# Optimization experiments

Measured on AMD Instinct MI355X. Metric: run time of the kernel, lower is better.

## Reference

```python
import jax, jax.numpy as jnp
import numpy as np

H = 32          # num query heads
KV = 8          # num kv heads
D = 64          # head_dim
WIN = 512       # sliding_window
BASE = 10000.0  # rope base


def setup_inputs() -> dict:
    key = jax.random.key(0)
    ks = jax.random.split(key, 5)
    B, S, DIM = 2, 2048, 2048
    x = jax.random.normal(ks[0], (B, S, DIM), dtype=jnp.float32)
    wq = jax.random.normal(ks[1], (H * D, DIM), dtype=jnp.float32) * 0.02
    wk = jax.random.normal(ks[2], (KV * D, DIM), dtype=jnp.float32) * 0.02
    wv = jax.random.normal(ks[3], (KV * D, DIM), dtype=jnp.float32) * 0.02
    wo = jax.random.normal(ks[4], (DIM, H * D), dtype=jnp.float32) * 0.02
    return {"x": x, "wq": wq, "wk": wk, "wv": wv, "wo": wo}


def _rope_tables(S):
    inv_freq = 1.0 / (BASE ** (jnp.arange(0, D, 2, dtype=jnp.float32) / D))
    t = jnp.arange(S, dtype=jnp.float32)
    freqs = t[:, None] * inv_freq[None, :]          # [S, D/2]
    emb = jnp.concatenate([freqs, freqs], axis=-1)  # [S, D]
    return jnp.cos(emb)[:, None, :], jnp.sin(emb)[:, None, :]  # [S,1,D]


def _rotate_half(u):
    return jnp.concatenate([-u[..., D // 2:], u[..., :D // 2]], axis=-1)


def reference(x, wq, wk, wv, wo):
    B, S, _ = x.shape
    q = (x @ wq.T).reshape(B, S, H, D)
    k = (x @ wk.T).reshape(B, S, KV, D)
    v = (x @ wv.T).reshape(B, S, KV, D)

    cos, sin = _rope_tables(S)  # [S,1,D] broadcasts over batch and heads
    q = q * cos + _rotate_half(q) * sin
    k = k * cos + _rotate_half(k) * sin

    q = q.transpose(0, 2, 1, 3)                        # [B,H,S,D]
    k = jnp.repeat(k.transpose(0, 2, 1, 3), H // KV, axis=1)  # [B,H,S,D]
    v = jnp.repeat(v.transpose(0, 2, 1, 3), H // KV, axis=1)

    scale = 1.0 / jnp.sqrt(jnp.float32(D))
    scores = jnp.einsum('bhqd,bhkd->bhqk', q, k) * scale  # [B,H,S,S]

    i = jnp.arange(S)[:, None]
    j = jnp.arange(S)[None, :]
    window_mask = jnp.abs(i - j) > WIN // 2   # True = masked (outside window)
    causal_mask = j > i                        # True = masked (future)
    masked = window_mask | causal_mask
    scores = jnp.where(masked[None, None], -jnp.inf, scores)

    attn = jax.nn.softmax(scores, axis=-1)
    out = jnp.einsum('bhqk,bhkd->bhqd', attn, v)  # [B,H,S,D]
    out = out.transpose(0, 2, 1, 3).reshape(B, S, H * D)
    return out @ wo.T
```

## Files before the change

kernel.cpp:

```cpp
#include <hip/hip_runtime.h>
#include <cstdint>
#include <cstddef>

#define SLEN 2048
#define NB 2
#define NH 32
#define NKV 8
#define HD 64
#define MROWS 4096
#define QDIM 2048
#define KVDIM 512
#define WINH 256

typedef float f32x4 __attribute__((ext_vector_type(4)));
typedef __bf16 bf16x8 __attribute__((ext_vector_type(8)));

__device__ __forceinline__ unsigned short f2bf(float f) {
  union { float f; unsigned u; } v; v.f = f;
  unsigned r = v.u + 0x7fffu + ((v.u >> 16) & 1u);
  return (unsigned short)(r >> 16);
}
__device__ __forceinline__ float bf2f(unsigned short h) {
  union { unsigned u; float f; } v; v.u = ((unsigned)h) << 16;
  return v.f;
}
__device__ __forceinline__ unsigned pk2(float a, float b) {
  return (unsigned)f2bf(a) | ((unsigned)f2bf(b) << 16);
}
__device__ __forceinline__ unsigned cvtpk(float a, float b) {
  unsigned r;
  asm("v_cvt_pk_bf16_f32 %0, %1, %2" : "=v"(r) : "v"(a), "v"(b));
  return r;
}
__device__ __forceinline__ uint4 cvt16(float4 a, float4 b) {
  uint4 u;
  u.x = pk2(a.x, a.y); u.y = pk2(a.z, a.w);
  u.z = pk2(b.x, b.y); u.w = pk2(b.z, b.w);
  return u;
}
__device__ __forceinline__ void async16(const unsigned short* g, unsigned short* l) {
  __builtin_amdgcn_global_load_lds(
      (const __attribute__((address_space(1))) unsigned int*)g,
      (__attribute__((address_space(3))) unsigned int*)l, 16, 0, 0);
}

__global__ void rope_table(float2* __restrict__ tab) {
  int tid = blockIdx.x * 256 + threadIdx.x;
  int d = tid & 31;
  int s = tid >> 5;
  float inv = expf((float)d * (-2.0f / 64.0f) * 9.210340371976184f);
  float ang = (float)s * inv;
  float sn, cs;
  sincosf(ang, &sn, &cs);
  tab[tid] = make_float2(cs, sn);
}

__global__ void conv_xw(const float* __restrict__ x,
                        const float* __restrict__ wq, const float* __restrict__ wk,
                        const float* __restrict__ wv,
                        unsigned short* __restrict__ xb, unsigned short* __restrict__ wqkvb) {
  size_t t = (size_t)blockIdx.x * 256 + threadIdx.x;
  if (t < (size_t)1048576) {
    size_t e = t * 8;
    float4 a = *(const float4*)(x + e);
    float4 b = *(const float4*)(x + e + 4);
    *(uint4*)(xb + e) = cvt16(a, b);
  } else {
    size_t e = (t - 1048576) * 8;
    int row = (int)(e >> 11);
    const float* src; size_t off;
    if (row < 2048)       { src = wq; off = e; }
    else if (row < 2560)  { src = wk; off = e - (size_t)2048 * 2048; }
    else                  { src = wv; off = e - (size_t)2560 * 2048; }
    float4 a = *(const float4*)(src + off);
    float4 b = *(const float4*)(src + off + 4);
    *(uint4*)(wqkvb + e) = cvt16(a, b);
  }
}

__global__ void conv_bf16(const float* __restrict__ src, unsigned short* __restrict__ dst) {
  size_t t = (size_t)blockIdx.x * 256 + threadIdx.x;
  float4 a = *(const float4*)(src + t * 8);
  float4 b = *(const float4*)(src + t * 8 + 4);
  *(uint4*)(dst + t * 8) = cvt16(a, b);
}

__global__ void rope_qk(unsigned short* __restrict__ qb,
                        unsigned short* __restrict__ kb,
                        const float* __restrict__ tabf) {
  const float2* tab = (const float2*)tabf;
  int tid = blockIdx.x * 256 + threadIdx.x;
  int oct = tid & 3;
  int head = (tid >> 2) % 40;
  int row = tid / 160;
  int s = row & (SLEN - 1);
  int d0 = oct * 8;
  unsigned short* p = (head < NH)
      ? qb + (size_t)row * QDIM + head * HD
      : kb + (size_t)row * KVDIM + (head - NH) * HD;
  uint4 u0 = *(const uint4*)(p + d0);
  uint4 u1 = *(const uint4*)(p + d0 + 32);
  const unsigned short* a16 = (const unsigned short*)&u0;
  const unsigned short* b16 = (const unsigned short*)&u1;
  unsigned short o0[8], o1[8];
#pragma unroll
  for (int j = 0; j < 8; ++j) {
    float2 cs = tab[s * 32 + d0 + j];
    float a = bf2f(a16[j]), b = bf2f(b16[j]);
    o0[j] = f2bf(a * cs.x - b * cs.y);
    o1[j] = f2bf(b * cs.x + a * cs.y);
  }
  *(uint4*)(p + d0)      = *(const uint4*)o0;
  *(uint4*)(p + d0 + 32) = *(const uint4*)o1;
}

__global__ __launch_bounds__(512, 2) void qkv_gemm(
    const unsigned short* __restrict__ Ap, const unsigned short* __restrict__ Bp,
    unsigned short* __restrict__ o_q, unsigned short* __restrict__ o_k,
    unsigned short* __restrict__ o_v)
{
  extern __shared__ unsigned short L[];
  constexpr int NT = 32;

  const int bid = blockIdx.x;
  const int swz = (bid & 7) * 32 + (bid >> 3);
  const int bm0 = (swz & 15) * 256;
  const int bn0 = (swz >> 4) * 192;

  const int tid = threadIdx.x;
  const int lane = tid & 63, wid = tid >> 6;
  const int g = lane >> 4, cl = lane & 15;
  const int wm = wid >> 2, wn = wid & 3;

  const int r0 = wid * 32 + (lane >> 2);
  const int s0 = (((lane & 3) ^ ((lane >> 3) & 3)) << 3);
  const unsigned short* gA = Ap + (size_t)(bm0 + r0) * 2048 + s0;
  const unsigned short* gB = Bp + (size_t)(bn0 + r0) * 2048 + s0;

  const int slotus = ((g ^ ((cl >> 1) & 3)) << 3);
  const int aread = (wm * 128 + cl) * 32 + slotus;
  const int bread = (wn * 48 + cl) * 32 + slotus;

#define REG_(b, op, kh) ((((b) * 2 + (op)) * 2 + (kh)) * 8192)
#define STG(op, kh, tt, db) do { \
    const unsigned short* s_ = ((op) ? gB : gA) + (tt) * 64 + (kh) * 32; \
    unsigned short* d_ = L + REG_(db, op, kh) + wid * 1024; \
    async16(s_, d_); \
    async16(s_ + 16 * 2048, d_ + 512); \
  } while (0)
#define LDA(dst, kh, mh) \
    _Pragma("unroll") for (int mf = 0; mf < 4; ++mf) \
      dst[mf] = *(const bf16x8*)&L[REG_(cb, 0, kh) + aread + (mh) * 2048 + mf * 512];
#define LDB(dst, kh) \
    _Pragma("unroll") for (int nf = 0; nf < 3; ++nf) \
      dst[nf] = *(const bf16x8*)&L[REG_(cb, 1, kh) + bread + nf * 512];
#define MM(mh, A, B) do { \
    __builtin_amdgcn_s_setprio(1); \
    _Pragma("unroll") for (int mf = 0; mf < 4; ++mf) \
      _Pragma("unroll") for (int nf = 0; nf < 3; ++nf) \
        acc[(mh) * 4 + mf][nf] = __builtin_amdgcn_mfma_f32_16x16x32_bf16( \
            A[mf], B[nf], acc[(mh) * 4 + mf][nf], 0, 0, 0); \
    __builtin_amdgcn_s_setprio(0); \
  } while (0)

  f32x4 acc[8][3] = {};

  STG(0, 0, 0, 0); STG(1, 0, 0, 0); STG(0, 1, 0, 0); STG(1, 1, 0, 0);
  STG(0, 0, 1, 1); STG(1, 0, 1, 1);
  asm volatile("s_waitcnt vmcnt(4)" ::: "memory");
  __builtin_amdgcn_s_barrier();
  __builtin_amdgcn_sched_barrier(0);

#pragma unroll 1
  for (int t = 0; t < NT; ++t) {
    const int cb = t & 1, nb = cb ^ 1;
    bf16x8 a00[4], a10[4], a01[4], a11[4], b0[3], b1[3];

    if (t + 1 < NT) STG(0, 1, t + 1, nb);
    LDA(a00, 0, 0); LDB(b0, 0);
    if (t + 1 < NT) STG(1, 1, t + 1, nb);
    LDA(a10, 0, 1);
    MM(0, a00, b0);
    LDA(a01, 1, 0); LDB(b1, 1);
    MM(1, a10, b0);
    asm volatile("s_waitcnt lgkmcnt(0)" ::: "memory");
    __builtin_amdgcn_s_barrier();
    __builtin_amdgcn_sched_barrier(0);
    if (t + 2 < NT) STG(0, 0, t + 2, cb);
    LDA(a11, 1, 1);
    MM(0, a01, b1);
    if (t + 2 < NT) STG(1, 0, t + 2, cb);
    MM(1, a11, b1);
    if (t + 2 < NT) { asm volatile("s_waitcnt vmcnt(4)" ::: "memory"); }
    else            { asm volatile("s_waitcnt vmcnt(0)" ::: "memory"); }
    asm volatile("s_waitcnt lgkmcnt(0)" ::: "memory");
    __builtin_amdgcn_s_barrier();
    __builtin_amdgcn_sched_barrier(0);
  }
#undef MM
#undef LDB
#undef LDA
#undef STG
#undef REG_

  const int rb = bm0 + wm * 128;
#pragma unroll
  for (int m = 0; m < 8; ++m)
#pragma unroll
    for (int nf = 0; nf < 3; ++nf) {
      const int col = bn0 + wn * 48 + nf * 16 + cl;
      if (col < QDIM) {
#pragma unroll
        for (int p = 0; p < 4; ++p) {
          int row = rb + m * 16 + g * 4 + p;
          o_q[(size_t)row * QDIM + col] = f2bf(acc[m][nf][p]);
        }
      } else if (col < QDIM + KVDIM) {
#pragma unroll
        for (int p = 0; p < 4; ++p) {
          int row = rb + m * 16 + g * 4 + p;
          o_k[(size_t)row * KVDIM + col - QDIM] = f2bf(acc[m][nf][p]);
        }
      } else {
        int vc = col - QDIM - KVDIM;
        int kvh = vc >> 6, d = vc & 63;
        int row0 = rb + m * 16 + g * 4;
        int bb = row0 >> 11, s = row0 & (SLEN - 1);
        unsigned short* dst = o_v + (((size_t)(bb * NKV + kvh) * HD + d) << 11) + s;
        uint2 u;
        u.x = pk2(acc[m][nf][0], acc[m][nf][1]);
        u.y = pk2(acc[m][nf][2], acc[m][nf][3]);
        *(uint2*)dst = u;
      }
    }
}

__global__ __launch_bounds__(512, 2) void out_gemm(
    const unsigned short* __restrict__ Ap, const unsigned short* __restrict__ Bp,
    float* __restrict__ o_f)
{
  extern __shared__ unsigned short L[];
  constexpr int NT = 32;

  const int bid = blockIdx.x;
  const int swz = (bid & 7) * 32 + (bid >> 3);
  const int bm0 = (swz & 31) * 128;
  const int bn0 = (swz >> 5) * 256;

  const int tid = threadIdx.x;
  const int lane = tid & 63, wid = tid >> 6;
  const int g = lane >> 4, cl = lane & 15;
  const int wm = wid >> 2, wn = wid & 3;

  const int s0 = (((lane & 3) ^ ((lane >> 3) & 3)) << 3);
  const unsigned short* gA = Ap + (size_t)(bm0 + wid * 16 + (lane >> 2)) * 2048 + s0;
  const unsigned short* gB = Bp + (size_t)(bn0 + wid * 32 + (lane >> 2)) * 2048 + s0;

  const int slotus = ((g ^ ((cl >> 1) & 3)) << 3);
  const int aread = (wm * 64 + cl) * 32 + slotus;
  const int bread = (wn * 64 + cl) * 32 + slotus;

#define REGA_(b, kh) ((b) * 24576 + (kh) * 4096)
#define REGB_(b, kh) ((b) * 24576 + 8192 + (kh) * 8192)
#define STGA(kh, tt, db) \
    async16(gA + (tt) * 64 + (kh) * 32, L + REGA_(db, kh) + wid * 512)
#define STGB(kh, tt, db) do { \
    const unsigned short* s_ = gB + (tt) * 64 + (kh) * 32; \
    unsigned short* d_ = L + REGB_(db, kh) + wid * 1024; \
    async16(s_, d_); \
    async16(s_ + 16 * 2048, d_ + 512); \
  } while (0)
#define LA(dst, kh, mp) \
    _Pragma("unroll") for (int mf = 0; mf < 2; ++mf) \
      dst[mf] = *(const bf16x8*)&L[REGA_(cb, kh) + aread + (mp) * 1024 + mf * 512];
#define LB(dst, kh) \
    _Pragma("unroll") for (int nf = 0; nf < 4; ++nf) \
      dst[nf] = *(const bf16x8*)&L[REGB_(cb, kh) + bread + nf * 512];
#define MMO(mp, A, B) do { \
    __builtin_amdgcn_s_setprio(1); \
    _Pragma("unroll") for (int mf = 0; mf < 2; ++mf) \
      _Pragma("unroll") for (int nf = 0; nf < 4; ++nf) \
        acc[(mp) * 2 + mf][nf] = __builtin_amdgcn_mfma_f32_16x16x32_bf16( \
            A[mf], B[nf], acc[(mp) * 2 + mf][nf], 0, 0, 0); \
    __builtin_amdgcn_s_setprio(0); \
  } while (0)

  f32x4 acc[4][4] = {};

  STGA(0, 0, 0); STGB(0, 0, 0); STGA(1, 0, 0); STGB(1, 0, 0);
  STGA(0, 1, 1); STGB(0, 1, 1);
  asm volatile("s_waitcnt vmcnt(3)" ::: "memory");
  __builtin_amdgcn_s_barrier();
  __builtin_amdgcn_sched_barrier(0);

#pragma unroll 1
  for (int t = 0; t < NT; ++t) {
    const int cb = t & 1, nb = cb ^ 1;
    bf16x8 p00[2], p10[2], p01[2], p11[2], b0[4], b1[4];

    if (t + 1 < NT) STGA(1, t + 1, nb);
    LA(p00, 0, 0); LB(b0, 0);
    if (t + 1 < NT) STGB(1, t + 1, nb);
    LA(p10, 0, 1);
    MMO(0, p00, b0);
    LA(p01, 1, 0); LB(b1, 1);
    MMO(1, p10, b0);
    asm volatile("s_waitcnt lgkmcnt(0)" ::: "memory");
    __builtin_amdgcn_s_barrier();
    __builtin_amdgcn_sched_barrier(0);
    if (t + 2 < NT) STGA(0, t + 2, cb);
    LA(p11, 1, 1);
    MMO(0, p01, b1);
    if (t + 2 < NT) STGB(0, t + 2, cb);
    MMO(1, p11, b1);
    if (t + 2 < NT) { asm volatile("s_waitcnt vmcnt(3)" ::: "memory"); }
    else            { asm volatile("s_waitcnt vmcnt(0)" ::: "memory"); }
    asm volatile("s_waitcnt lgkmcnt(0)" ::: "memory");
    __builtin_amdgcn_s_barrier();
    __builtin_amdgcn_sched_barrier(0);
  }
#undef MMO
#undef LB
#undef LA
#undef STGB
#undef STGA
#undef REGB_
#undef REGA_

  const int rb = bm0 + wm * 64;
  const int colb = bn0 + wn * 64;
#pragma unroll
  for (int m = 0; m < 4; ++m)
#pragma unroll
    for (int nf = 0; nf < 4; ++nf)
#pragma unroll
      for (int p = 0; p < 4; ++p) {
        int row = rb + m * 16 + g * 4 + p;
        o_f[(size_t)row * 2048 + colb + nf * 16 + cl] = acc[m][nf][p];
      }
}

__global__ __launch_bounds__(256) void attn(
    const unsigned short* __restrict__ qb, const unsigned short* __restrict__ kb,
    const unsigned short* __restrict__ vt, unsigned short* __restrict__ ao)
{
  __shared__ __align__(16) unsigned short Plds[4][2][16][40];
  const int lane = threadIdx.x & 63, wid = threadIdx.x >> 6;
  const int g = lane >> 4, cl = lane & 15;
  const int qt = blockIdx.x * 4 + wid;
  const int bh = qt >> 6, tl = qt & 63;
  const int i0 = tl * 32;
  const int b = bh >> 5, h = bh & 31, kvh = (bh & 31) >> 2;
  const int qi0 = i0 + cl, qi1 = i0 + 16 + cl;

  const unsigned short* qp0 = qb + ((size_t)(b * SLEN + qi0) * NH + h) * HD + g * 8;
  const unsigned short* qp1 = qb + ((size_t)(b * SLEN + qi1) * NH + h) * HD + g * 8;
  bf16x8 qf00 = *(const bf16x8*)qp0, qf01 = *(const bf16x8*)(qp0 + 32);
  bf16x8 qf10 = *(const bf16x8*)qp1, qf11 = *(const bf16x8*)(qp1 + 32);

  const unsigned short* kbase = kb + ((size_t)b * SLEN * NKV + kvh) * HD + g * 8;
  const unsigned short* vbase = vt + ((size_t)(b * NKV + kvh) * HD) * SLEN;

  f32x4 acc0[4] = {}, acc1[4] = {};
  float m0 = -1e30f, l0 = 0.f, m1 = -1e30f, l1 = 0.f;
  const int jb = (i0 > WINH) ? (i0 - WINH) : 0;

#define LOADK(dst, jj) do { \
    _Pragma("unroll") for (int t = 0; t < 2; ++t) { \
      int krow = (jj) + 16 * t + cl; \
      if (krow > SLEN - 1) krow = SLEN - 1; \
      const unsigned short* kp_ = kbase + (size_t)krow * KVDIM; \
      dst[t * 2]     = *(const bf16x8*)kp_; \
      dst[t * 2 + 1] = *(const bf16x8*)(kp_ + 32); \
    } \
  } while (0)

#define LOADV(dst, jj) do { \
    int jv = (jj) + g * 8; \
    if (jv > SLEN - 8) jv = SLEN - 8; \
    _Pragma("unroll") for (int vb2 = 0; vb2 < 4; ++vb2) \
      dst[vb2] = *(const bf16x8*)(vbase + (size_t)(vb2 * 16 + cl) * SLEN + jv); \
  } while (0)

#define SOFTMAX(SAC, MR, LR, ACC, QI, QF) do { \
    float sm[2][4]; float mx = -1e30f; \
    _Pragma("unroll") for (int t = 0; t < 2; ++t) \
      _Pragma("unroll") for (int p = 0; p < 4; ++p) { \
        int kj = j0 + 16 * t + 4 * g + p; \
        bool ok = (kj <= (QI)) && ((QI) - kj <= WINH); \
        float v = ok ? SAC[t][p] * 0.125f : -1e30f; \
        sm[t][p] = v; mx = fmaxf(mx, v); \
      } \
    mx = fmaxf(mx, __shfl_xor(mx, 16)); \
    mx = fmaxf(mx, __shfl_xor(mx, 32)); \
    float mnew = fmaxf(MR, mx); \
    float corr = __expf(MR - mnew); \
    float ps = 0.f; unsigned pw00, pw01, pw10, pw11; \
    { \
      float p0 = __expf(sm[0][0] - mnew), p1 = __expf(sm[0][1] - mnew); \
      float p2 = __expf(sm[0][2] - mnew), p3 = __expf(sm[0][3] - mnew); \
      ps += p0 + p1 + p2 + p3; pw00 = cvtpk(p0, p1); pw01 = cvtpk(p2, p3); \
      float p4 = __expf(sm[1][0] - mnew), p5 = __expf(sm[1][1] - mnew); \
      float p6 = __expf(sm[1][2] - mnew), p7 = __expf(sm[1][3] - mnew); \
      ps += p4 + p5 + p6 + p7; pw10 = cvtpk(p4, p5); pw11 = cvtpk(p6, p7); \
    } \
    ps += __shfl_xor(ps, 16); ps += __shfl_xor(ps, 32); \
    LR = LR * corr + ps; MR = mnew; \
    _Pragma("unroll") for (int vb2 = 0; vb2 < 4; ++vb2) \
      _Pragma("unroll") for (int p = 0; p < 4; ++p) ACC[vb2][p] *= corr; \
    *(unsigned*)&Plds[wid][QF][cl][4 * g]          = pw00; \
    *(unsigned*)&Plds[wid][QF][cl][4 * g + 2]      = pw01; \
    *(unsigned*)&Plds[wid][QF][cl][16 + 4 * g]     = pw10; \
    *(unsigned*)&Plds[wid][QF][cl][16 + 4 * g + 2] = pw11; \
  } while (0)

#define BODY(KC, KN, VC, VN) do { \
    LOADK(KN, j0 + 32);                           \
    LOADV(VN, j0 + 32);                           \
    f32x4 s0[2], s1[2]; \
    _Pragma("unroll") for (int t = 0; t < 2; ++t) { \
      f32x4 z = {}; \
      z = __builtin_amdgcn_mfma_f32_16x16x32_bf16(KC[t * 2], qf00, z, 0, 0, 0); \
      z = __builtin_amdgcn_mfma_f32_16x16x32_bf16(KC[t * 2 + 1], qf01, z, 0, 0, 0); \
      s0[t] = z; \
      f32x4 z2 = {}; \
      z2 = __builtin_amdgcn_mfma_f32_16x16x32_bf16(KC[t * 2], qf10, z2, 0, 0, 0); \
      z2 = __builtin_amdgcn_mfma_f32_16x16x32_bf16(KC[t * 2 + 1], qf11, z2, 0, 0, 0); \
      s1[t] = z2; \
    } \
    SOFTMAX(s0, m0, l0, acc0, qi0, 0); \
    SOFTMAX(s1, m1, l1, acc1, qi1, 1); \
    bf16x8 pf0 = *(const bf16x8*)&Plds[wid][0][cl][g * 8]; \
    bf16x8 pf1 = *(const bf16x8*)&Plds[wid][1][cl][g * 8]; \
    _Pragma("unroll") for (int vb2 = 0; vb2 < 4; ++vb2) \
      acc0[vb2] = __builtin_amdgcn_mfma_f32_16x16x32_bf16(VC[vb2], pf0, acc0[vb2], 0, 0, 0); \
    _Pragma("unroll") for (int vb2 = 0; vb2 < 4; ++vb2) \
      acc1[vb2] = __builtin_amdgcn_mfma_f32_16x16x32_bf16(VC[vb2], pf1, acc1[vb2], 0, 0, 0); \
  } while (0)

  bf16x8 kA[4], kB[4], vA[4], vB[4];
  LOADK(kA, jb); LOADV(vA, jb);
  int j0 = jb;
  for (;;) {
    BODY(kA, kB, vA, vB); j0 += 32; if (j0 > i0) break;
    BODY(kB, kA, vB, vA); j0 += 32; if (j0 > i0) break;
  }
#undef BODY
#undef SOFTMAX
#undef LOADV
#undef LOADK

  float inv0 = 1.0f / l0, inv1 = 1.0f / l1;
  unsigned short* op0 = ao + ((size_t)(b * SLEN + qi0) * NH + h) * HD;
  unsigned short* op1 = ao + ((size_t)(b * SLEN + qi1) * NH + h) * HD;
#pragma unroll
  for (int vbk = 0; vbk < 4; ++vbk) {
    *(unsigned*)(op0 + vbk * 16 + g * 4)     = cvtpk(acc0[vbk][0] * inv0, acc0[vbk][1] * inv0);
    *(unsigned*)(op0 + vbk * 16 + g * 4 + 2) = cvtpk(acc0[vbk][2] * inv0, acc0[vbk][3] * inv0);
    *(unsigned*)(op1 + vbk * 16 + g * 4)     = cvtpk(acc1[vbk][0] * inv1, acc1[vbk][1] * inv1);
    *(unsigned*)(op1 + vbk * 16 + g * 4 + 2) = cvtpk(acc1[vbk][2] * inv1, acc1[vbk][3] * inv1);
  }
}

extern "C" void kernel_launch(void* const* d_in, const int* in_sizes, int n_in,
                              void* d_out, int out_size, void* d_ws, size_t ws_size,
                              hipStream_t stream) {
  const float* x  = (const float*)d_in[0];
  const float* wq = (const float*)d_in[1];
  const float* wk = (const float*)d_in[2];
  const float* wv = (const float*)d_in[3];
  const float* wo = (const float*)d_in[4];
  float* out = (float*)d_out;

  char* w = (char*)d_ws;
  unsigned short* wqkvb = (unsigned short*)w; w += (size_t)3136 * 2048 * 2;
  unsigned short* xb    = (unsigned short*)w; w += (size_t)MROWS * QDIM * 2;
  unsigned short* qb    = (unsigned short*)w; w += (size_t)MROWS * QDIM * 2;
  unsigned short* kb    = (unsigned short*)w; w += (size_t)MROWS * KVDIM * 2;
  unsigned short* vt    = (unsigned short*)w; w += (size_t)MROWS * KVDIM * 2;
  float* tab            = (float*)w;          w += (size_t)SLEN * 32 * 8;
  unsigned short* wob = wqkvb;
  unsigned short* ao  = xb;

  hipFuncSetAttribute((const void*)qkv_gemm,
                      hipFuncAttributeMaxDynamicSharedMemorySize, 131072);
  hipFuncSetAttribute((const void*)out_gemm,
                      hipFuncAttributeMaxDynamicSharedMemorySize, 98304);

  rope_table<<<SLEN * 32 / 256, 256, 0, stream>>>((float2*)tab);
  conv_xw<<<7168, 256, 0, stream>>>(x, wq, wk, wv, xb, wqkvb);
  qkv_gemm<<<256, 512, 131072, stream>>>(xb, wqkvb, qb, kb, vt);
  rope_qk<<<(MROWS * 40 * 4) / 256, 256, 0, stream>>>(qb, kb, tab);
  conv_bf16<<<(2048 * 2048) / (8 * 256), 256, 0, stream>>>(wo, wob);
  attn<<<(NB * NH * (SLEN / 32)) / 4, 256, 0, stream>>>(qb, kb, vt, ao);
  out_gemm<<<256, 512, 98304, stream>>>(ao, wob, out);
}
```

Before: 168.0 us.

## Software-pipeline attention QK^T ahead of softmax, fuse rope table into conversion

The attention inner loop is restructured so the QK^T MFMAs for the next 32-key block are issued before the softmax and PV of the current block, with K loads prefetched two blocks ahead. This lets matrix work overlap the exp and shuffle latency of the softmax. The rope table kernel is folded into the conv_xw launch as extra threads, removing one kernel launch. A sched_barrier is also removed from both GEMM main loops, giving the compiler more freedom to schedule, at the cost of higher register pressure and possibly a worse instruction order.

```diff
diff --git a/kernel.cpp b/kernel.cpp
--- a/kernel.cpp
+++ b/kernel.cpp
@@ -44,28 +44,18 @@
       (__attribute__((address_space(3))) unsigned int*)l, 16, 0, 0);
 }
 
-__global__ void rope_table(float2* __restrict__ tab) {
-  int tid = blockIdx.x * 256 + threadIdx.x;
-  int d = tid & 31;
-  int s = tid >> 5;
-  float inv = expf((float)d * (-2.0f / 64.0f) * 9.210340371976184f);
-  float ang = (float)s * inv;
-  float sn, cs;
-  sincosf(ang, &sn, &cs);
-  tab[tid] = make_float2(cs, sn);
-}
-
 __global__ void conv_xw(const float* __restrict__ x,
                         const float* __restrict__ wq, const float* __restrict__ wk,
                         const float* __restrict__ wv,
-                        unsigned short* __restrict__ xb, unsigned short* __restrict__ wqkvb) {
+                        unsigned short* __restrict__ xb, unsigned short* __restrict__ wqkvb,
+                        float2* __restrict__ tab) {
   size_t t = (size_t)blockIdx.x * 256 + threadIdx.x;
   if (t < (size_t)1048576) {
     size_t e = t * 8;
     float4 a = *(const float4*)(x + e);
     float4 b = *(const float4*)(x + e + 4);
     *(uint4*)(xb + e) = cvt16(a, b);
-  } else {
+  } else if (t < (size_t)1835008) {
     size_t e = (t - 1048576) * 8;
     int row = (int)(e >> 11);
     const float* src; size_t off;
@@ -75,6 +65,15 @@
     float4 a = *(const float4*)(src + off);
     float4 b = *(const float4*)(src + off + 4);
     *(uint4*)(wqkvb + e) = cvt16(a, b);
+  } else {
+    int id = (int)(t - 1835008);
+    int d = id & 31;
+    int s = id >> 5;
+    float inv = expf((float)d * (-2.0f / 64.0f) * 9.210340371976184f);
+    float ang = (float)s * inv;
+    float sn, cs;
+    sincosf(ang, &sn, &cs);
+    tab[id] = make_float2(cs, sn);
   }
 }
 
@@ -185,7 +184,6 @@
     MM(1, a10, b0);
     asm volatile("s_waitcnt lgkmcnt(0)" ::: "memory");
     __builtin_amdgcn_s_barrier();
-    __builtin_amdgcn_sched_barrier(0);
     if (t + 2 < NT) STG(0, 0, t + 2, cb);
     LDA(a11, 1, 1);
     MM(0, a01, b1);
@@ -307,7 +305,6 @@
     MMO(1, p10, b0);
     asm volatile("s_waitcnt lgkmcnt(0)" ::: "memory");
     __builtin_amdgcn_s_barrier();
-    __builtin_amdgcn_sched_barrier(0);
     if (t + 2 < NT) STGA(0, t + 2, cb);
     LA(p11, 1, 1);
     MMO(0, p01, b1);
@@ -380,6 +377,19 @@
     if (jv > SLEN - 8) jv = SLEN - 8; \
     _Pragma("unroll") for (int vb2 = 0; vb2 < 4; ++vb2) \
       dst[vb2] = *(const bf16x8*)(vbase + (size_t)(vb2 * 16 + cl) * SLEN + jv); \
+  } while (0)
+
+#define QKT(S0, S1, KK) do { \
+    _Pragma("unroll") for (int t = 0; t < 2; ++t) { \
+      f32x4 z = {}; \
+      z = __builtin_amdgcn_mfma_f32_16x16x32_bf16(KK[t * 2], qf00, z, 0, 0, 0); \
+      z = __builtin_amdgcn_mfma_f32_16x16x32_bf16(KK[t * 2 + 1], qf01, z, 0, 0, 0); \
+      S0[t] = z; \
+      f32x4 z2 = {}; \
+      z2 = __builtin_amdgcn_mfma_f32_16x16x32_bf16(KK[t * 2], qf10, z2, 0, 0, 0); \
+      z2 = __builtin_amdgcn_mfma_f32_16x16x32_bf16(KK[t * 2 + 1], qf11, z2, 0, 0, 0); \
+      S1[t] = z2; \
+    } \
   } while (0)
 
 #define SOFTMAX(SAC, MR, LR, ACC, QI, QF) do { \
@@ -414,39 +424,47 @@
     *(unsigned*)&Plds[wid][QF][cl][16 + 4 * g + 2] = pw11; \
   } while (0)
 
-#define BODY(KC, KN, VC, VN) do { \
-    LOADK(KN, j0 + 32);                           \
-    LOADV(VN, j0 + 32);                           \
-    f32x4 s0[2], s1[2]; \
-    _Pragma("unroll") for (int t = 0; t < 2; ++t) { \
-      f32x4 z = {}; \
-      z = __builtin_amdgcn_mfma_f32_16x16x32_bf16(KC[t * 2], qf00, z, 0, 0, 0); \
-      z = __builtin_amdgcn_mfma_f32_16x16x32_bf16(KC[t * 2 + 1], qf01, z, 0, 0, 0); \
-      s0[t] = z; \
-      f32x4 z2 = {}; \
-      z2 = __builtin_amdgcn_mfma_f32_16x16x32_bf16(KC[t * 2], qf10, z2, 0, 0, 0); \
-      z2 = __builtin_amdgcn_mfma_f32_16x16x32_bf16(KC[t * 2 + 1], qf11, z2, 0, 0, 0); \
-      s1[t] = z2; \
-    } \
-    SOFTMAX(s0, m0, l0, acc0, qi0, 0); \
-    SOFTMAX(s1, m1, l1, acc1, qi1, 1); \
+#define PV(VV) do { \
     bf16x8 pf0 = *(const bf16x8*)&Plds[wid][0][cl][g * 8]; \
     bf16x8 pf1 = *(const bf16x8*)&Plds[wid][1][cl][g * 8]; \
     _Pragma("unroll") for (int vb2 = 0; vb2 < 4; ++vb2) \
-      acc0[vb2] = __builtin_amdgcn_mfma_f32_16x16x32_bf16(VC[vb2], pf0, acc0[vb2], 0, 0, 0); \
+      acc0[vb2] = __builtin_amdgcn_mfma_f32_16x16x32_bf16(VV[vb2], pf0, acc0[vb2], 0, 0, 0); \
     _Pragma("unroll") for (int vb2 = 0; vb2 < 4; ++vb2) \
-      acc1[vb2] = __builtin_amdgcn_mfma_f32_16x16x32_bf16(VC[vb2], pf1, acc1[vb2], 0, 0, 0); \
+      acc1[vb2] = __builtin_amdgcn_mfma_f32_16x16x32_bf16(VV[vb2], pf1, acc1[vb2], 0, 0, 0); \
   } while (0)
 
   bf16x8 kA[4], kB[4], vA[4], vB[4];
+  f32x4 sA0[2], sA1[2], sB0[2], sB1[2];
+
   LOADK(kA, jb); LOADV(vA, jb);
+  QKT(sA0, sA1, kA);
+  LOADK(kB, jb + 32);
   int j0 = jb;
   for (;;) {
-    BODY(kA, kB, vA, vB); j0 += 32; if (j0 > i0) break;
-    BODY(kB, kA, vB, vA); j0 += 32; if (j0 > i0) break;
+    {
+      bool more = (j0 + 32 <= i0);
+      if (more) LOADV(vB, j0 + 32);
+      if (j0 + 64 <= i0) LOADK(kA, j0 + 64);
+      if (more) QKT(sB0, sB1, kB);
+      SOFTMAX(sA0, m0, l0, acc0, qi0, 0);
+      SOFTMAX(sA1, m1, l1, acc1, qi1, 1);
+      PV(vA);
+      j0 += 32; if (!more) break;
+    }
+    {
+      bool more = (j0 + 32 <= i0);
+      if (more) LOADV(vA, j0 + 32);
+      if (j0 + 64 <= i0) LOADK(kB, j0 + 64);
+      if (more) QKT(sA0, sA1, kA);
+      SOFTMAX(sB0, m0, l0, acc0, qi0, 0);
+      SOFTMAX(sB1, m1, l1, acc1, qi1, 1);
+      PV(vB);
+      j0 += 32; if (!more) break;
+    }
   }
-#undef BODY
+#undef PV
 #undef SOFTMAX
+#undef QKT
 #undef LOADV
 #undef LOADK
 
@@ -487,8 +505,7 @@
   hipFuncSetAttribute((const void*)out_gemm,
                       hipFuncAttributeMaxDynamicSharedMemorySize, 98304);
 
-  rope_table<<<SLEN * 32 / 256, 256, 0, stream>>>((float2*)tab);
-  conv_xw<<<7168, 256, 0, stream>>>(x, wq, wk, wv, xb, wqkvb);
+  conv_xw<<<7424, 256, 0, stream>>>(x, wq, wk, wv, xb, wqkvb, (float2*)tab);
   qkv_gemm<<<256, 512, 131072, stream>>>(xb, wqkvb, qb, kb, vt);
   rope_qk<<<(MROWS * 40 * 4) / 256, 256, 0, stream>>>(qb, kb, tab);
   conv_bf16<<<(2048 * 2048) / (8 * 256), 256, 0, stream>>>(wo, wob);
```

Result: slower. 181.4 us (+8.0%).
